# Optimization experiments

Measured on AMD Instinct MI355X. Metric: run time of the kernel, lower is better.

Reference implementation:

```python
import jax, jax.numpy as jnp
import numpy as np
from math import sqrt

ROPE_BASE = 6000.0


def _rope_tables(seq_len, rope_dim, dtype):
    # inv_freq: [rope_dim/2]; emb = concat(freqs, freqs) along last dim -> [seq_len, rope_dim]
    inv_freq = 1.0 / (ROPE_BASE ** (jnp.arange(0, rope_dim, 2, dtype=jnp.float32) / rope_dim))
    t = jnp.arange(seq_len, dtype=jnp.float32)
    freqs = jnp.outer(t, inv_freq)
    emb = jnp.concatenate([freqs, freqs], axis=-1)
    return jnp.cos(emb).astype(dtype), jnp.sin(emb).astype(dtype)


def _rotate_half(x):
    x1, x2 = jnp.split(x, 2, axis=-1)
    return jnp.concatenate([-x2, x1], axis=-1)


def setup_inputs() -> dict:
    key = jax.random.key(0)
    k1, k2, k3 = jax.random.split(key, 3)
    B, S, D = 2, 2048, 1024
    H, DK = 16, 64
    x = jax.random.normal(k1, (B, S, D), dtype=jnp.float32)
    W_qkv = jax.random.normal(k2, (3, H, DK, D), dtype=jnp.float32) * 0.02
    W_o = jax.random.normal(k3, (D, H * DK), dtype=jnp.float32) * 0.02
    return {"x": x, "W_qkv": W_qkv, "W_o": W_o}


def reference(x, W_qkv, W_o):
    B, S, D = x.shape
    _, H, DK, _ = W_qkv.shape
    rope_dim = DK // 2  # RotaryEmbeddings(dim=d_k // 2)

    # fused QKV projection: [B, 3, H, S, DK]
    qkv = jnp.einsum('bsm,qhdm->bqhsd', x, W_qkv)

    # inline RoPE on Q and K, first rope_dim channels only
    cos, sin = _rope_tables(S, rope_dim, x.dtype)  # [S, rope_dim]
    qk = qkv[:, :2, :, :, :rope_dim]
    qk_rot = qk * cos + _rotate_half(qk) * sin
    qkv = qkv.at[:, :2, :, :, :rope_dim].set(qk_rot)

    Q, K, V = qkv[:, 0], qkv[:, 1], qkv[:, 2]  # [B, H, S, DK]

    scores = jnp.einsum('bhqd,bhkd->bhqk', Q, K)
    causal = jnp.triu(jnp.ones((S, S), dtype=bool), k=1)
    scores = jnp.where(causal, -jnp.inf, scores) / sqrt(DK)
    attn = jax.nn.softmax(scores, axis=-1)
    out = jnp.einsum('bhqk,bhkd->bhqd', attn, V)

    # concat heads: [B, S, H*DK], then output projection (Linear weight [D, H*DK])
    out = out.transpose(0, 2, 1, 3).reshape(B, S, H * DK)
    return jnp.einsum('bsh,dh->bsd', out, W_o)
```

## Files before the change

kernel.cpp:

```cpp
#include <hip/hip_runtime.h>
#include <math.h>


static constexpr int Bb  = 2;
static constexpr int Ss  = 2048;
static constexpr int Hh  = 16;
static constexpr int DKk = 64;

static constexpr size_t QSZ = (size_t)Bb * Hh * Ss * DKk;

static constexpr size_t WOB_E  = 0;
static constexpr size_t XB_E   = 1048576;
static constexpr size_t WQKV_E = 5242880;
static constexpr size_t QB_E   = 9437184;
static constexpr size_t OB_E   = QB_E + 3*QSZ;
static constexpr size_t OP_BYTE = 2097152;
static constexpr size_t LP_BYTE = 52428800;

typedef __attribute__((ext_vector_type(8))) short short8;
typedef __attribute__((ext_vector_type(4))) float f32x4;

__device__ __forceinline__ unsigned short f2bf(float f) {
    unsigned int u = __float_as_uint(f);
    u += 0x7fffu + ((u >> 16) & 1u);
    return (unsigned short)(u >> 16);
}

__device__ __forceinline__ unsigned int pk_hu(float lo, float hi) {
    const unsigned int ul = __float_as_uint(lo) + 0x8000u;
    const unsigned int uh = __float_as_uint(hi) + 0x8000u;
    return (uh & 0xffff0000u) | (ul >> 16);
}

__device__ __forceinline__ float fexp2(float x) {
    float r;
    asm("v_exp_f32 %0, %1" : "=v"(r) : "v"(x));
    return r;
}

__device__ __forceinline__ float fsin_rev(float r) {
    float o;
    asm("v_sin_f32 %0, %1" : "=v"(o) : "v"(r));
    return o;
}
__device__ __forceinline__ float fcos_rev(float r) {
    float o;
    asm("v_cos_f32 %0, %1" : "=v"(o) : "v"(r));
    return o;
}

__device__ __forceinline__ void gl16(const unsigned short* g, unsigned short* l) {
    __builtin_amdgcn_global_load_lds(
        (const __attribute__((address_space(1))) void*)g,
        (__attribute__((address_space(3))) void*)l, 16, 0, 0);
}

__global__ __launch_bounds__(256)
void convert_bf16(const float* __restrict__ x, const float* __restrict__ wqkv,
                  const float* __restrict__ wo, unsigned short* __restrict__ dst,
                  float* __restrict__ Lp)
{
    if (blockIdx.x >= 8192) {
        const size_t j4 = ((size_t)(blockIdx.x - 8192) * 256 + threadIdx.x) * 4;
        *(float4*)(Lp + j4) = float4{0.f, 0.f, 0.f, 0.f};
        return;
    }
    const size_t i4 = ((size_t)blockIdx.x * 256 + threadIdx.x) * 4;
    const float* src;
    if (i4 < 1048576)      src = wo   + i4;
    else if (i4 < 5242880) src = x    + (i4 - 1048576);
    else                   src = wqkv + (i4 - 5242880);
    const float4 v = *(const float4*)src;
    ushort4 p = { f2bf(v.x), f2bf(v.y), f2bf(v.z), f2bf(v.w) };
    *(ushort4*)(dst + i4) = p;
}

template<int MODE, int BN>
__global__ __launch_bounds__(256)
void gemm_mfma(const unsigned short* __restrict__ A,
               const unsigned short* __restrict__ Bm,
               float* __restrict__ C, unsigned short* __restrict__ QKV, int N)
{
    constexpr int K  = 1024;
    constexpr int NF = BN / 32;
    __shared__ unsigned short As0[128 * 32];
    __shared__ unsigned short As1[128 * 32];
    __shared__ unsigned short Bs0[BN * 32];
    __shared__ unsigned short Bs1[BN * 32];

    const int t    = threadIdx.x;
    const int lane = t & 63;
    const int w    = t >> 6;
    const int l15  = lane & 15;
    const int quad = lane >> 4;
    const int wr   = w >> 1;
    const int wc   = w & 1;
    const int n0   = blockIdx.x * BN;
    const int m0   = blockIdx.y * 128;

    const unsigned short* Ag = A  + (size_t)(m0 + (t >> 2)) * K + (t & 3) * 8;
    const unsigned short* Bg = Bm + (size_t)(n0 + (t >> 2)) * K + (t & 3) * 8;

    f32x4 acc[4][NF];
    #pragma unroll
    for (int i = 0; i < 4; i++)
        #pragma unroll
        for (int j = 0; j < NF; j++) acc[i][j] = f32x4{0.f, 0.f, 0.f, 0.f};

    auto stage = [&](int k0, unsigned short* Asb, unsigned short* Bsb) {
        gl16(Ag + k0,        Asb + t*8);
        gl16(Ag + 64*K + k0, Asb + 2048 + t*8);
        gl16(Bg + k0,        Bsb + t*8);
        if (BN == 128) gl16(Bg + 64*K + k0, Bsb + 2048 + t*8);
    };
    auto comp = [&](const unsigned short* Asb, const unsigned short* Bsb) {
        short8 af[4], bfv[NF];
        #pragma unroll
        for (int mf = 0; mf < 4; mf++)
            af[mf] = *(const short8*)&Asb[(wr*64 + mf*16 + l15) * 32 + quad*8];
        #pragma unroll
        for (int nf = 0; nf < NF; nf++)
            bfv[nf] = *(const short8*)&Bsb[(wc*(BN/2) + nf*16 + l15) * 32 + quad*8];
        #pragma unroll
        for (int mf = 0; mf < 4; mf++)
            #pragma unroll
            for (int nf = 0; nf < NF; nf++)
                acc[mf][nf] = __builtin_amdgcn_mfma_f32_16x16x32_bf16(
                    af[mf], bfv[nf], acc[mf][nf], 0, 0, 0);
    };

    stage(0, As0, Bs0);
    for (int k0 = 0; k0 < K; k0 += 64) {
        __syncthreads();
        stage(k0 + 32, As1, Bs1);
        comp(As0, Bs0);
        __syncthreads();
        if (k0 + 64 < K) stage(k0 + 64, As0, Bs0);
        comp(As1, Bs1);
    }

    if (MODE == 0) {
        #pragma unroll
        for (int mf = 0; mf < 4; mf++)
            #pragma unroll
            for (int r = 0; r < 4; r++) {
                float* crow = C + (size_t)(m0 + wr*64 + mf*16 + quad*4 + r) * N
                            + n0 + wc*(BN/2);
                #pragma unroll
                for (int nf = 0; nf < NF; nf++)
                    crow[nf*16 + l15] = acc[mf][nf][r];
            }
    } else {
        const int col0 = n0 + wc*64;
        const int q    = col0 >> 10;
        const int h    = (col0 >> 6) & 15;
        const int row0 = m0 + wr*64;
        const int b    = row0 >> 11;
        const int s0   = row0 & 2047;
        if (q == 2) {
            #pragma unroll
            for (int mf = 0; mf < 4; mf++) {
                const int sb = s0 + mf*16 + quad*4;
                #pragma unroll
                for (int nf = 0; nf < 4; nf++) {
                    const int d = nf*16 + l15;
                    ushort4 p = { f2bf(acc[mf][nf][0]), f2bf(acc[mf][nf][1]),
                                  f2bf(acc[mf][nf][2]), f2bf(acc[mf][nf][3]) };
                    *(ushort4*)(QKV + 2*QSZ
                        + ((size_t)((b*Hh + h) * DKk + d)) * Ss + sb) = p;
                }
            }
        } else {
            const float qsc = (q == 0) ? 0.125f * 1.44269504088896f : 1.0f;
            const float rev_freq = (float)(exp(-(double)(2 * l15) / 32.0
                                   * log(6000.0)) / 6.283185307179586);
            unsigned short* base = QKV + (size_t)q * QSZ
                                 + ((size_t)(b*Hh + h) * Ss) * DKk;
            #pragma unroll
            for (int mf = 0; mf < 4; mf++)
                #pragma unroll
                for (int r = 0; r < 4; r++) {
                    const int s = s0 + mf*16 + quad*4 + r;
                    float rev = (float)s * rev_freq;
                    rev -= floorf(rev);
                    const float sn = fsin_rev(rev);
                    const float cs = fcos_rev(rev);
                    const float v0 = acc[mf][0][r] * qsc;
                    const float v1 = acc[mf][1][r] * qsc;
                    unsigned short* rowp = base + (size_t)s * DKk;
                    rowp[l15]      = f2bf(v0 * cs - v1 * sn);
                    rowp[16 + l15] = f2bf(v1 * cs + v0 * sn);
                    rowp[32 + l15] = f2bf(acc[mf][2][r] * qsc);
                    rowp[48 + l15] = f2bf(acc[mf][3][r] * qsc);
                }
        }
    }
}

__global__ __launch_bounds__(256)
void flash_mfma(const unsigned short* __restrict__ Qa,
                const unsigned short* __restrict__ Ka,
                const unsigned short* __restrict__ Va,
                float* __restrict__ Op, float* __restrict__ Lp)
{
    __shared__ unsigned short Ks0[64*64];
    __shared__ unsigned short Ks1[64*64];
    __shared__ unsigned short Vs0[64*64];
    __shared__ unsigned short Vs1[64*64];

    const int t    = threadIdx.x;
    const int lane = t & 63;
    const int w    = t >> 6;
    const int l15  = lane & 15;
    const int quad = lane >> 4;

    const int bid   = blockIdx.x;
    const int xcd   = bid & 7;
    const int slot  = bid >> 3;
    const int start = xcd*1088 + (slot < 64 ? 9*slot : 576 + 8*(slot - 64));
    const int n     = (slot < 64) ? 9 : 8;

    int bh  = start / 272;
    int rem = start - bh*272;
    int QT  = 0;
    while ((QT+1)*(QT+2) <= rem) QT++;
    int kt  = rem - QT*(QT+1);

    const int c0 = t,       r0 = c0 >> 3, g0 = ((c0 & 7) ^ (r0 & 7)) * 8;
    const int c1 = t + 256, r1 = c1 >> 3, g1 = ((c1 & 7) ^ (r1 & 7)) * 8;

    auto stage = [&](int sbh, int skt, unsigned short* Ksb, unsigned short* Vsb) {
        const unsigned short* Kg = Ka + (size_t)sbh * Ss * DKk + (size_t)skt*64*DKk;
        const unsigned short* Vg = Va + (size_t)sbh * DKk * Ss + skt*64;
        gl16(Kg + (size_t)r0*DKk + g0, Ksb + t*8);
        gl16(Kg + (size_t)r1*DKk + g1, Ksb + (t+256)*8);
        gl16(Vg + (size_t)r0*Ss  + g0, Vsb + t*8);
        gl16(Vg + (size_t)r1*Ss  + g1, Vsb + (t+256)*8);
    };

    short8 qf[2][2];
    f32x4 o[2][4];
    float lacc[2];
    auto zero_acc = [&]() {
        #pragma unroll
        for (int mfq = 0; mfq < 2; mfq++) {
            lacc[mfq] = 0.f;
            #pragma unroll
            for (int i = 0; i < 4; i++) o[mfq][i] = f32x4{0.f,0.f,0.f,0.f};
        }
    };
    auto loadQ = [&](int qbh, int qQT) {
        #pragma unroll
        for (int mfq = 0; mfq < 2; mfq++) {
            const unsigned short* qrow = Qa + (size_t)qbh * Ss * DKk
                + (size_t)(qQT*128 + w*32 + mfq*16 + l15) * DKk;
            qf[mfq][0] = *(const short8*)(qrow + quad*8);
            qf[mfq][1] = *(const short8*)(qrow + 32 + quad*8);
        }
    };
    auto flush = [&](int obh, int oQT) {
        const int b = obh >> 4, h = obh & 15;
        const int q0 = oQT*128 + w*32;
        #pragma unroll
        for (int mfq = 0; mfq < 2; mfq++) {
            float ls = lacc[mfq];
            ls += __shfl_xor(ls, 16);
            ls += __shfl_xor(ls, 32);
            if (quad == 0)
                atomicAdd(&Lp[(size_t)obh*Ss + q0 + mfq*16 + l15], ls);
            #pragma unroll
            for (int r = 0; r < 4; r++) {
                const int row = q0 + mfq*16 + quad*4 + r;
                float* orow = Op + ((size_t)b*Ss + row) * 1024 + h*64;
                #pragma unroll
                for (int dt = 0; dt < 4; dt++)
                    atomicAdd(&orow[dt*16 + l15], o[mfq][dt][r]);
            }
        }
    };
    auto compute = [&](const unsigned short* Ksb, const unsigned short* Vsb,
                       int cQT, int ckt) {
        f32x4 sc[4][2];
        #pragma unroll
        for (int nt = 0; nt < 4; nt++)
            #pragma unroll
            for (int mfq = 0; mfq < 2; mfq++) sc[nt][mfq] = f32x4{0.f,0.f,0.f,0.f};
        #pragma unroll
        for (int nt = 0; nt < 4; nt++)
            #pragma unroll
            for (int kc = 0; kc < 2; kc++) {
                const short8 kf = *(const short8*)&Ksb[(nt*16 + l15)*64
                                   + (((kc*4 + quad) ^ (l15 & 7)) * 8)];
                sc[nt][0] = __builtin_amdgcn_mfma_f32_16x16x32_bf16(kf, qf[0][kc], sc[nt][0], 0,0,0);
                sc[nt][1] = __builtin_amdgcn_mfma_f32_16x16x32_bf16(kf, qf[1][kc], sc[nt][1], 0,0,0);
            }

        if (ckt >= 2*cQT) {
            const int kb = ckt*64 + quad*4;
            const int qb = cQT*128 + w*32 + l15;
            #pragma unroll
            for (int nt = 0; nt < 4; nt++)
                #pragma unroll
                for (int mfq = 0; mfq < 2; mfq++)
                    #pragma unroll
                    for (int r = 0; r < 4; r++)
                        if (kb + nt*16 + r > qb + mfq*16)
                            sc[nt][mfq][r] = -INFINITY;
        }

        #pragma unroll
        for (int nt = 0; nt < 4; nt++)
            #pragma unroll
            for (int mfq = 0; mfq < 2; mfq++)
                #pragma unroll
                for (int r = 0; r < 4; r++)
                    sc[nt][mfq][r] = fexp2(sc[nt][mfq][r]);
        #pragma unroll
        for (int mfq = 0; mfq < 2; mfq++)
            #pragma unroll
            for (int nt = 0; nt < 4; nt++)
                lacc[mfq] += (sc[nt][mfq][0] + sc[nt][mfq][1])
                           + (sc[nt][mfq][2] + sc[nt][mfq][3]);

        short8 pfrag[2][2];
        #pragma unroll
        for (int mfq = 0; mfq < 2; mfq++)
            #pragma unroll
            for (int kc = 0; kc < 2; kc++) {
                unsigned int pk[4];
                #pragma unroll
                for (int v = 0; v < 4; v++) {
                    const int nt = 2*kc + (v >> 1);
                    const int rr = 2*(v & 1);
                    pk[v] = pk_hu(sc[nt][mfq][rr], sc[nt][mfq][rr+1]);
                }
                pfrag[mfq][kc] = *(short8*)&pk[0];
            }

        #pragma unroll
        for (int dt = 0; dt < 4; dt++) {
            const int row = dt*16 + l15;
            const int rx  = row & 7;
            const int wi  = 4*(quad & 1);
            #pragma unroll
            for (int kc = 0; kc < 2; kc++) {
                const ushort4 lo = *(const ushort4*)&Vsb[row*64
                                    + (((4*kc + (quad>>1)) ^ rx) * 8) + wi];
                const ushort4 hi = *(const ushort4*)&Vsb[row*64
                                    + (((4*kc + 2 + (quad>>1)) ^ rx) * 8) + wi];
                short8 vf;
                vf[0]=lo.x; vf[1]=lo.y; vf[2]=lo.z; vf[3]=lo.w;
                vf[4]=hi.x; vf[5]=hi.y; vf[6]=hi.z; vf[7]=hi.w;
                o[0][dt] = __builtin_amdgcn_mfma_f32_16x16x32_bf16(
                    pfrag[0][kc], vf, o[0][dt], 0,0,0);
                o[1][dt] = __builtin_amdgcn_mfma_f32_16x16x32_bf16(
                    pfrag[1][kc], vf, o[1][dt], 0,0,0);
            }
        }
    };

    int cbh = bh, cQT = QT, ckt = kt;
    int pbh = bh, pQT = QT, pkt = kt;
    auto advance = [&]() {
        pkt++;
        if (pkt == 2*pQT + 2) { pkt = 0; pQT++; if (pQT == 16) { pQT = 0; pbh++; } }
    };

    stage(pbh, pkt, Ks0, Vs0);
    advance();
    int own_bh = cbh, own_QT = cQT;
    loadQ(own_bh, own_QT);
    zero_acc();

    int i = 0;
    while (true) {
        __syncthreads();
        const bool h1 = (i + 1 < n);
        if (h1) stage(pbh, pkt, Ks1, Vs1);
        if (cbh != own_bh || cQT != own_QT) {
            flush(own_bh, own_QT); zero_acc();
            own_bh = cbh; own_QT = cQT; loadQ(own_bh, own_QT);
        }
        compute(Ks0, Vs0, cQT, ckt);
        if (!h1) break;
        cbh = pbh; cQT = pQT; ckt = pkt; advance();
        i++;
        __syncthreads();
        const bool h2 = (i + 1 < n);
        if (h2) stage(pbh, pkt, Ks0, Vs0);
        if (cbh != own_bh || cQT != own_QT) {
            flush(own_bh, own_QT); zero_acc();
            own_bh = cbh; own_QT = cQT; loadQ(own_bh, own_QT);
        }
        compute(Ks1, Vs1, cQT, ckt);
        if (!h2) break;
        cbh = pbh; cQT = pQT; ckt = pkt; advance();
        i++;
    }
    flush(own_bh, own_QT);
}

__global__ __launch_bounds__(256)
void reduce_o(const float* __restrict__ Op, const float* __restrict__ Lp,
              unsigned short* __restrict__ Ob)
{
    const size_t i4 = ((size_t)blockIdx.x * 256 + threadIdx.x) * 4;
    const int row = (int)(i4 >> 10);
    const int col = (int)(i4 & 1023);
    const int h   = col >> 6;
    const int b   = row >> 11;
    const int s   = row & 2047;
    const float inv = 1.0f / Lp[(size_t)((b << 4) + h) * Ss + s];
    const float4 v = *(const float4*)(Op + i4);
    ushort4 p = { f2bf(v.x*inv), f2bf(v.y*inv), f2bf(v.z*inv), f2bf(v.w*inv) };
    *(ushort4*)(Ob + i4) = p;
}

extern "C" void kernel_launch(void* const* d_in, const int* in_sizes, int n_in,
                              void* d_out, int out_size, void* d_ws, size_t ws_size,
                              hipStream_t stream)
{
    const float* x    = (const float*)d_in[0];
    const float* Wqkv = (const float*)d_in[1];
    const float* Wo   = (const float*)d_in[2];
    float* out = (float*)d_out;
    unsigned short* wsu = (unsigned short*)d_ws;
    float* Op = (float*)((char*)d_ws + OP_BYTE);
    float* Lp = (float*)((char*)d_ws + LP_BYTE);

    const dim3 blk(256);
    convert_bf16<<<dim3(8256), blk, 0, stream>>>(x, Wqkv, Wo, wsu, Lp);
    gemm_mfma<1,128><<<dim3(24, 32), blk, 0, stream>>>(wsu + XB_E, wsu + WQKV_E,
                                                       nullptr, wsu + QB_E, 3072);
    hipMemsetAsync((char*)d_ws + OP_BYTE, 0, 16777216, stream);
    flash_mfma<<<dim3(1024), blk, 0, stream>>>(wsu + QB_E, wsu + QB_E + QSZ,
                                               wsu + QB_E + 2*QSZ, Op, Lp);
    reduce_o<<<dim3(4096), blk, 0, stream>>>(Op, Lp, wsu + OB_E);
    gemm_mfma<0,64><<<dim3(16, 32), blk, 0, stream>>>(wsu + OB_E, wsu + WOB_E,
                                                      out, nullptr, 1024);
}
```

Before: 208.4 us.

## Triple-buffer K/V tiles with vmcnt waits and raise MFMA wave priority

Result: no change. 212.0 us (+1.7%).

```diff
diff --git a/kernel.cpp b/kernel.cpp
--- a/kernel.cpp
+++ b/kernel.cpp
@@ -203,10 +203,8 @@
                 const unsigned short* __restrict__ Va,
                 float* __restrict__ Op, float* __restrict__ Lp)
 {
-    __shared__ unsigned short Ks0[64*64];
-    __shared__ unsigned short Ks1[64*64];
-    __shared__ unsigned short Vs0[64*64];
-    __shared__ unsigned short Vs1[64*64];
+    __shared__ unsigned short KsA[3][64*64];
+    __shared__ unsigned short VsA[3][64*64];
 
     const int t    = threadIdx.x;
     const int lane = t & 63;
@@ -285,6 +283,7 @@
         for (int nt = 0; nt < 4; nt++)
             #pragma unroll
             for (int mfq = 0; mfq < 2; mfq++) sc[nt][mfq] = f32x4{0.f,0.f,0.f,0.f};
+        __builtin_amdgcn_s_setprio(1);
         #pragma unroll
         for (int nt = 0; nt < 4; nt++)
             #pragma unroll
@@ -294,6 +293,7 @@
                 sc[nt][0] = __builtin_amdgcn_mfma_f32_16x16x32_bf16(kf, qf[0][kc], sc[nt][0], 0,0,0);
                 sc[nt][1] = __builtin_amdgcn_mfma_f32_16x16x32_bf16(kf, qf[1][kc], sc[nt][1], 0,0,0);
             }
+        __builtin_amdgcn_s_setprio(0);
 
         if (ckt >= 2*cQT) {
             const int kb = ckt*64 + quad*4;
@@ -337,6 +337,7 @@
                 pfrag[mfq][kc] = *(short8*)&pk[0];
             }
 
+        __builtin_amdgcn_s_setprio(1);
         #pragma unroll
         for (int dt = 0; dt < 4; dt++) {
             const int row = dt*16 + l15;
@@ -357,45 +358,39 @@
                     pfrag[1][kc], vf, o[1][dt], 0,0,0);
             }
         }
+        __builtin_amdgcn_s_setprio(0);
     };
 
     int cbh = bh, cQT = QT, ckt = kt;
     int pbh = bh, pQT = QT, pkt = kt;
-    auto advance = [&]() {
+    auto advc = [&]() {
+        ckt++;
+        if (ckt == 2*cQT + 2) { ckt = 0; cQT++; if (cQT == 16) { cQT = 0; cbh++; } }
+    };
+    auto advp = [&]() {
         pkt++;
         if (pkt == 2*pQT + 2) { pkt = 0; pQT++; if (pQT == 16) { pQT = 0; pbh++; } }
     };
 
-    stage(pbh, pkt, Ks0, Vs0);
-    advance();
+    stage(pbh, pkt, KsA[0], VsA[0]); advp();
+    if (n > 1) { stage(pbh, pkt, KsA[1], VsA[1]); advp(); }
     int own_bh = cbh, own_QT = cQT;
     loadQ(own_bh, own_QT);
     zero_acc();
 
-    int i = 0;
-    while (true) {
-        __syncthreads();
-        const bool h1 = (i + 1 < n);
-        if (h1) stage(pbh, pkt, Ks1, Vs1);
+    for (int i = 0; i < n; i++) {
+        if (i + 1 < n) asm volatile("s_waitcnt vmcnt(4)" ::: "memory");
+        else           asm volatile("s_waitcnt vmcnt(0)" ::: "memory");
+        __builtin_amdgcn_s_barrier();
+        __builtin_amdgcn_sched_barrier(0);
+        const int cur = i % 3;
+        if (i + 2 < n) { stage(pbh, pkt, KsA[(i+2)%3], VsA[(i+2)%3]); advp(); }
         if (cbh != own_bh || cQT != own_QT) {
             flush(own_bh, own_QT); zero_acc();
             own_bh = cbh; own_QT = cQT; loadQ(own_bh, own_QT);
         }
-        compute(Ks0, Vs0, cQT, ckt);
-        if (!h1) break;
-        cbh = pbh; cQT = pQT; ckt = pkt; advance();
-        i++;
-        __syncthreads();
-        const bool h2 = (i + 1 < n);
-        if (h2) stage(pbh, pkt, Ks0, Vs0);
-        if (cbh != own_bh || cQT != own_QT) {
-            flush(own_bh, own_QT); zero_acc();
-            own_bh = cbh; own_QT = cQT; loadQ(own_bh, own_QT);
-        }
-        compute(Ks1, Vs1, cQT, ckt);
-        if (!h2) break;
-        cbh = pbh; cQT = pQT; ckt = pkt; advance();
-        i++;
+        compute(KsA[cur], VsA[cur], cQT, ckt);
+        advc();
     }
     flush(own_bh, own_QT);
 }
```

## Stage transposed V epilogue through LDS and use hardware bf16 pack

Applied to the files above, without the earlier changes.

Result: faster. 203.7 us (-2.3%).

```diff
diff --git a/kernel.cpp b/kernel.cpp
--- a/kernel.cpp
+++ b/kernel.cpp
@@ -26,10 +26,10 @@
     return (unsigned short)(u >> 16);
 }
 
-__device__ __forceinline__ unsigned int pk_hu(float lo, float hi) {
-    const unsigned int ul = __float_as_uint(lo) + 0x8000u;
-    const unsigned int uh = __float_as_uint(hi) + 0x8000u;
-    return (uh & 0xffff0000u) | (ul >> 16);
+__device__ __forceinline__ unsigned int cvtpk_bf16(float lo, float hi) {
+    unsigned int r;
+    asm("v_cvt_pk_bf16_f32 %0, %1, %2" : "=v"(r) : "v"(lo), "v"(hi));
+    return r;
 }
 
 __device__ __forceinline__ float fexp2(float x) {
@@ -81,12 +81,15 @@
                const unsigned short* __restrict__ Bm,
                float* __restrict__ C, unsigned short* __restrict__ QKV, int N)
 {
-    constexpr int K  = 1024;
-    constexpr int NF = BN / 32;
-    __shared__ unsigned short As0[128 * 32];
-    __shared__ unsigned short As1[128 * 32];
-    __shared__ unsigned short Bs0[BN * 32];
-    __shared__ unsigned short Bs1[BN * 32];
+    constexpr int K   = 1024;
+    constexpr int NF  = BN / 32;
+    constexpr int ASZ = 128 * 32;
+    constexpr int BSZ = BN * 32;
+    __shared__ unsigned short ShPool[2 * ASZ + 2 * BSZ];
+    unsigned short* As0 = ShPool;
+    unsigned short* As1 = ShPool + ASZ;
+    unsigned short* Bs0 = ShPool + 2 * ASZ;
+    unsigned short* Bs1 = ShPool + 2 * ASZ + BSZ;
 
     const int t    = threadIdx.x;
     const int lane = t & 63;
@@ -151,6 +154,7 @@
                     crow[nf*16 + l15] = acc[mf][nf][r];
             }
     } else {
+        __syncthreads();
         const int col0 = n0 + wc*64;
         const int q    = col0 >> 10;
         const int h    = (col0 >> 6) & 15;
@@ -158,16 +162,30 @@
         const int b    = row0 >> 11;
         const int s0   = row0 & 2047;
         if (q == 2) {
-            #pragma unroll
-            for (int mf = 0; mf < 4; mf++) {
-                const int sb = s0 + mf*16 + quad*4;
-                #pragma unroll
-                for (int nf = 0; nf < 4; nf++) {
-                    const int d = nf*16 + l15;
-                    ushort4 p = { f2bf(acc[mf][nf][0]), f2bf(acc[mf][nf][1]),
-                                  f2bf(acc[mf][nf][2]), f2bf(acc[mf][nf][3]) };
-                    *(ushort4*)(QKV + 2*QSZ
-                        + ((size_t)((b*Hh + h) * DKk + d)) * Ss + sb) = p;
+            unsigned short* chunk = ShPool + w * 2048;
+            unsigned short* vb = QKV + 2*QSZ
+                               + (size_t)(b*Hh + h) * DKk * Ss + s0;
+            #pragma unroll
+            for (int pass = 0; pass < 2; pass++) {
+                #pragma unroll
+                for (int mf = 0; mf < 4; mf++)
+                    #pragma unroll
+                    for (int nfp = 0; nfp < 2; nfp++) {
+                        const int nf = pass*2 + nfp;
+                        const int dl = nfp*16 + l15;
+                        const int sby = (mf*16 + quad*4) * 2;
+                        ushort4 pv = { f2bf(acc[mf][nf][0]), f2bf(acc[mf][nf][1]),
+                                       f2bf(acc[mf][nf][2]), f2bf(acc[mf][nf][3]) };
+                        *(ushort4*)((char*)chunk
+                            + dl*128 + (sby ^ ((dl & 7) << 4))) = pv;
+                    }
+                #pragma unroll
+                for (int dblk = 0; dblk < 8; dblk++) {
+                    const int dl = dblk*4 + quad;
+                    const int sl = l15*4;
+                    const ushort4 pv = *(const ushort4*)((char*)chunk
+                        + dl*128 + ((sl*2) ^ ((dl & 7) << 4)));
+                    *(ushort4*)(vb + (size_t)(pass*32 + dl) * Ss + sl) = pv;
                 }
             }
         } else {
@@ -332,7 +350,7 @@
                 for (int v = 0; v < 4; v++) {
                     const int nt = 2*kc + (v >> 1);
                     const int rr = 2*(v & 1);
-                    pk[v] = pk_hu(sc[nt][mfq][rr], sc[nt][mfq][rr+1]);
+                    pk[v] = cvtpk_bf16(sc[nt][mfq][rr], sc[nt][mfq][rr+1]);
                 }
                 pfrag[mfq][kc] = *(short8*)&pk[0];
             }
```
